# Optimization experiments

Hardware: AMD Instinct MI355X
Metric: run time of the kernel (lower is better)

The kernel has to match this reference:

```python
import jax, jax.numpy as jnp
import numpy as np

W = 128; H = 128; NEAR = 0.1; FAR = 10.0; EPS = 1e-8
B = 1; V = 512; F = 1024


def _perspective(cf, cc):
    # OpenGL-convention projection, returned transposed for row-vector multiply
    f = 0.5 * (cf[0] + cf[1]); pco = 0.5
    right = (W - (cc[0] + pco)) * (NEAR / f)
    left = -(cc[0] + pco) * (NEAR / f)
    top = (cc[1] + pco) * (NEAR / f)
    bottom = -(H - cc[1] + pco) * (NEAR / f)
    z = jnp.zeros(())
    m = jnp.stack([
        jnp.stack([2.0 * NEAR / (right - left), z, (right + left) / (right - left), z]),
        jnp.stack([z, 2.0 * NEAR / (top - bottom), (top + bottom) / (top - bottom), z]),
        jnp.stack([z, z, jnp.full((), -(FAR + NEAR) / (FAR - NEAR)), jnp.full((), -2.0 * FAR * NEAR / (FAR - NEAR))]),
        jnp.stack([z, z, jnp.full((), -1.0), z]),
    ])
    return m.T


def _rodrigues(r):
    theta = jnp.sqrt(jnp.sum(r * r) + 1e-12)
    k = r / theta
    zz = jnp.zeros(())
    K = jnp.stack([
        jnp.stack([zz, -k[2], k[1]]),
        jnp.stack([k[2], zz, -k[0]]),
        jnp.stack([-k[1], k[0], zz]),
    ])
    return jnp.eye(3) + jnp.sin(theta) * K + (1.0 - jnp.cos(theta)) * (K @ K)


def _view_matrix(rt, t):
    # row-vector convention: v' = v @ M, M = rodrigues^T composed with translation-in-last-row
    R = _rodrigues(rt)
    Mr = jnp.eye(4).at[:3, :3].set(R.T)
    Mt = jnp.eye(4).at[3, :3].set(t)
    return Mr @ Mt


def _rasterize_one(vs_xy, z_ndc, inv_w, valid_tri, f, vc, bgcolor, px, py):
    # vs_xy [V,2] screen coords, z_ndc [V], inv_w [V]; f [F,3] int; pixels px,py [P]
    a = vs_xy[f[:, 0]]; b = vs_xy[f[:, 1]]; c = vs_xy[f[:, 2]]  # [F,2]
    x = px[:, None]; y = py[:, None]  # [P,1]
    def E(p, q):  # signed edge function, broadcast to [P,F]
        return (q[:, 0] - p[:, 0]) * (y - p[:, 1]) - (q[:, 1] - p[:, 1]) * (x - p[:, 0])
    w0 = E(b, c); w1 = E(c, a); w2 = E(a, b)  # [P,F]
    area = (b[:, 0] - a[:, 0]) * (c[:, 1] - a[:, 1]) - (b[:, 1] - a[:, 1]) * (c[:, 0] - a[:, 0])  # [F]
    area_safe = jnp.where(jnp.abs(area) > EPS, area, 1.0)
    b0 = w0 / area_safe; b1 = w1 / area_safe; b2 = w2 / area_safe
    za = z_ndc[f[:, 0]]; zb = z_ndc[f[:, 1]]; zc = z_ndc[f[:, 2]]
    z = b0 * za + b1 * zb + b2 * zc  # [P,F] interpolated NDC depth
    inside = ((b0 >= 0) & (b1 >= 0) & (b2 >= 0) & (jnp.abs(area) > EPS)
              & valid_tri[None, :] & (z >= -1.0) & (z <= 1.0))
    depth = jnp.where(inside, z, jnp.inf)
    best = jnp.argmin(depth, axis=1)  # [P] z-buffer winner
    covered = jnp.take_along_axis(depth, best[:, None], 1)[:, 0] <= 1.0
    take = lambda m: jnp.take_along_axis(m, best[:, None], 1)[:, 0]
    bs = jnp.stack([take(b0), take(b1), take(b2)], -1)  # [P,3]
    tri = f[best]          # [P,3]
    iw = inv_w[tri]        # [P,3]
    col = vc[tri]          # [P,3,C]
    den = jnp.sum(bs * iw, -1)
    den = jnp.where(jnp.abs(den) > EPS, den, 1.0)
    color = jnp.einsum('pk,pk,pkc->pc', bs, iw, col) / den[:, None]  # perspective-correct
    return jnp.where(covered[:, None], color, bgcolor[None, :])  # [P,C]


def reference(v, vc, f, bgcolor, camera_f, camera_c, camera_t, camera_rt):
    view = _view_matrix(camera_rt, camera_t)
    proj = _perspective(camera_f, camera_c)
    vh = jnp.concatenate([v, jnp.ones_like(v[..., :1])], -1)  # [B,V,4]
    clip = vh @ (view @ proj)                                 # [B,V,4]
    wc = clip[..., 3]
    valid_v = wc > EPS                                        # in front of camera
    w_safe = jnp.where(valid_v, wc, 1.0)
    ndc = clip[..., :3] / w_safe[..., None]
    xs = (ndc[..., 0] * 0.5 + 0.5) * W
    ys = (0.5 - ndc[..., 1] * 0.5) * H
    vs_xy = jnp.stack([xs, ys], -1)                           # [B,V,2]
    inv_w = 1.0 / w_safe
    valid_tri = valid_v[:, f].all(-1)                         # [B,F]
    gy, gx = jnp.meshgrid(jnp.arange(H, dtype=jnp.float32) + 0.5,
                          jnp.arange(W, dtype=jnp.float32) + 0.5, indexing='ij')
    px = gx.reshape(-1); py = gy.reshape(-1)
    img = jax.vmap(lambda xy, zn, iw, vt: _rasterize_one(xy, zn, iw, vt, f, vc, bgcolor, px, py))(
        vs_xy, ndc[..., 2], inv_w, valid_tri)
    return img.reshape(v.shape[0], H, W, vc.shape[-1])


def setup_inputs() -> dict:
    key = jax.random.key(0)
    k1, k2, k3 = jax.random.split(key, 3)
    u = jax.random.uniform(k1, (B, V, 3), dtype=jnp.float32)
    # x,y in [-0.8,0.8], z in [-3,-1] (camera looks along -z)
    vtx = jnp.stack([u[..., 0] * 1.6 - 0.8, u[..., 1] * 1.6 - 0.8, -(1.0 + 2.0 * u[..., 2])], -1)
    vc = jax.random.uniform(k2, (V, 3), dtype=jnp.float32)
    f = jax.random.randint(k3, (F, 3), 0, V, dtype=jnp.int32)
    return {
        'v': vtx,
        'vc': vc,
        'f': f,
        'bgcolor': jnp.zeros((3,), jnp.float32),
        'camera_f': jnp.array([128.0, 128.0], jnp.float32),
        'camera_c': jnp.array([64.0, 64.0], jnp.float32),
        'camera_t': jnp.zeros((3,), jnp.float32),
        'camera_rt': jnp.zeros((3,), jnp.float32),
    }
```

## Files before the change

kernel.cpp:

```cpp
#include <hip/hip_runtime.h>
#include <math.h>
#include <stdint.h>

#define NV 512
#define NF 1024
#define TRI_STRIDE 16
#define TRI_CHUNK 64
#define NCHUNK (NF / TRI_CHUNK)


__global__ __launch_bounds__(1024) void setup_kernel(
    const float* __restrict__ v, const int* __restrict__ fidx,
    const float* __restrict__ camf, const float* __restrict__ camc,
    const float* __restrict__ camt, const float* __restrict__ camrt,
    double* __restrict__ vdata, double* __restrict__ tridata,
    unsigned long long* __restrict__ keys)
{
#pragma clang fp contract(off)
  __shared__ double sM[16];
  __shared__ double sxs[NV], sys_[NV], szn[NV];
  __shared__ int svld[NV];
  const int tid = threadIdx.x;

  for (int i = tid; i < 16384; i += 1024) keys[i] = ~0ull;

  if (tid == 0) {
    float r0f = camrt[0], r1f = camrt[1], r2f = camrt[2];
    float th = sqrtf(((r0f * r0f + r1f * r1f) + r2f * r2f) + 1e-12f);
    float k0 = r0f / th, k1 = r1f / th, k2 = r2f / th;
    float sthf = sinf(th);
    float cthf = 1.0f - cosf(th);
    double K[3][3] = {{0.0, -(double)k2, (double)k1},
                      {(double)k2, 0.0, -(double)k0},
                      {-(double)k1, (double)k0, 0.0}};
    double KK[3][3];
    for (int i = 0; i < 3; ++i)
      for (int j = 0; j < 3; ++j)
        KK[i][j] = (K[i][0] * K[0][j] + K[i][1] * K[1][j]) + K[i][2] * K[2][j];
    double R[3][3];
    for (int i = 0; i < 3; ++i)
      for (int j = 0; j < 3; ++j) {
        double e = (i == j) ? 1.0 : 0.0;
        R[i][j] = (e + (double)sthf * K[i][j]) + (double)cthf * KK[i][j];
      }
    double Mr[4][4], Mt[4][4];
    for (int i = 0; i < 4; ++i)
      for (int j = 0; j < 4; ++j) {
        Mr[i][j] = (i == j) ? 1.0 : 0.0;
        Mt[i][j] = (i == j) ? 1.0 : 0.0;
      }
    for (int i = 0; i < 3; ++i)
      for (int j = 0; j < 3; ++j) Mr[i][j] = R[j][i];
    Mt[3][0] = (double)camt[0]; Mt[3][1] = (double)camt[1]; Mt[3][2] = (double)camt[2];
    double view[4][4];
    for (int i = 0; i < 4; ++i)
      for (int j = 0; j < 4; ++j)
        view[i][j] = ((Mr[i][0] * Mt[0][j] + Mr[i][1] * Mt[1][j]) +
                      Mr[i][2] * Mt[2][j]) + Mr[i][3] * Mt[3][j];
    float fcam = 0.5f * (camf[0] + camf[1]);
    float nf = 0.1f / fcam;
    float ccx = camc[0], ccy = camc[1];
    float right = (128.0f - (ccx + 0.5f)) * nf;
    float left = -(ccx + 0.5f) * nf;
    float top = (ccy + 0.5f) * nf;
    float bottom = -((128.0f - ccy) + 0.5f) * nf;
    float m00f = 0.2f / (right - left);
    float m02f = (right + left) / (right - left);
    float m11f = 0.2f / (top - bottom);
    float m12f = (top + bottom) / (top - bottom);
    double P[4][4] = {
        {(double)m00f, 0.0, (double)m02f, 0.0},
        {0.0, (double)m11f, (double)m12f, 0.0},
        {0.0, 0.0, -(10.0 + 0.1) / (10.0 - 0.1),
         -2.0 * 10.0 * 0.1 / (10.0 - 0.1)},
        {0.0, 0.0, -1.0, 0.0}};
    for (int i = 0; i < 4; ++i)
      for (int j = 0; j < 4; ++j)
        sM[i * 4 + j] = ((view[i][0] * P[j][0] + view[i][1] * P[j][1]) +
                         view[i][2] * P[j][2]) + view[i][3] * P[j][3];
  }
  __syncthreads();

  if (tid < NV) {
    double x = (double)v[tid * 3 + 0];
    double y = (double)v[tid * 3 + 1];
    double zz = (double)v[tid * 3 + 2];
    double c0 = ((x * sM[0] + y * sM[4]) + zz * sM[8]) + sM[12];
    double c1 = ((x * sM[1] + y * sM[5]) + zz * sM[9]) + sM[13];
    double c2 = ((x * sM[2] + y * sM[6]) + zz * sM[10]) + sM[14];
    double c3 = ((x * sM[3] + y * sM[7]) + zz * sM[11]) + sM[15];
    int valid = c3 > 1e-8;
    double wsafe = valid ? c3 : 1.0;
    double n0 = c0 / wsafe, n1 = c1 / wsafe, n2 = c2 / wsafe;
    double xs = (n0 * 0.5 + 0.5) * 128.0;
    double ys = (0.5 - n1 * 0.5) * 128.0;
    double iw = 1.0 / wsafe;
    sxs[tid] = xs; sys_[tid] = ys; szn[tid] = n2; svld[tid] = valid;
    vdata[0 * NV + tid] = xs;
    vdata[1 * NV + tid] = ys;
    vdata[2 * NV + tid] = n2;
    vdata[3 * NV + tid] = iw;
  }
  __syncthreads();

  {
    int i0 = fidx[tid * 3 + 0], i1 = fidx[tid * 3 + 1], i2 = fidx[tid * 3 + 2];
    double ax = sxs[i0], ay = sys_[i0];
    double bx = sxs[i1], by = sys_[i1];
    double cx = sxs[i2], cy = sys_[i2];
    double p1 = (bx - ax) * (cy - ay);
    double p2 = (by - ay) * (cx - ax);
    double area = p1 - p2;
    bool ok = (fabs(area) > 1e-8) && svld[i0] && svld[i1] && svld[i2];
    double s = (area > 0.0) ? 1.0 : -1.0;
    double inv_abs = ok ? s / area : 1.0;
    double bad = ok ? 0.0 : __builtin_nan("");
    double* td = tridata + tid * TRI_STRIDE;
    td[0] = bx;  td[1] = by;  td[2] = cx;  td[3] = cy;  td[4] = ax;  td[5] = ay;
    td[6] = s * (cx - bx) + bad;  td[7] = s * (cy - by) + bad;
    td[8] = s * (ax - cx) + bad;  td[9] = s * (ay - cy) + bad;
    td[10] = s * (bx - ax) + bad; td[11] = s * (by - ay) + bad;
    td[12] = szn[i0] * inv_abs;
    td[13] = szn[i1] * inv_abs;
    td[14] = szn[i2] * inv_abs;
    td[15] = inv_abs;
  }
}

__global__ __launch_bounds__(256) void raster_kernel(
    const double* __restrict__ tridata, unsigned long long* __restrict__ keys)
{
  __shared__ double st[15][TRI_CHUNK];
  const int tid = threadIdx.x;
  const int chunk = blockIdx.y;
  for (int i = tid; i < 15 * TRI_CHUNK; i += 256) {
    int fld = i >> 6, t = i & 63;
    st[fld][t] = tridata[(chunk * TRI_CHUNK + t) * TRI_STRIDE + fld];
  }
  __syncthreads();

  const int tile = blockIdx.x;
  const int x = ((tile & 7) << 4) + (tid & 15);
  const int y = ((tile >> 3) << 4) + (tid >> 4);
  const double px = (double)x + 0.5, py = (double)y + 0.5;

  double bestz = INFINITY;
  unsigned int bestt = 0;
  for (int t = 0; t < TRI_CHUNK; ++t) {
    double w0 = st[6][t] * (py - st[1][t]) - st[7][t] * (px - st[0][t]);
    double w1 = st[8][t] * (py - st[3][t]) - st[9][t] * (px - st[2][t]);
    double w2 = st[10][t] * (py - st[5][t]) - st[11][t] * (px - st[4][t]);
    double z = (w0 * st[12][t] + w1 * st[13][t]) + w2 * st[14][t];
    bool ins = (w0 >= 0.0) & (w1 >= 0.0) & (w2 >= 0.0) &
               (z >= -1.0) & (z <= 1.0) & (z < bestz);
    if (ins) { bestz = z; bestt = (unsigned int)t; }
  }
  if (bestz < INFINITY) {
    unsigned long long zq = (unsigned long long)((bestz + 1.0) * 4503599627370496.0);
    unsigned long long key = (zq << 10) | (unsigned long long)(chunk * TRI_CHUNK + bestt);
    atomicMin(&keys[y * 128 + x], key);
  }
}

__global__ __launch_bounds__(256) void color_kernel(
    const unsigned long long* __restrict__ keys,
    const double* __restrict__ vdata, const double* __restrict__ tridata,
    const int* __restrict__ fidx, const float* __restrict__ vc,
    const float* __restrict__ bg, float* __restrict__ out)
{
  const int p = blockIdx.x * 256 + threadIdx.x;
  if (p >= 16384) return;
  const int x = p & 127, y = p >> 7;
  unsigned long long key = keys[p];
  float cr, cg, cb;
  if (key == ~0ull) {
    cr = bg[0]; cg = bg[1]; cb = bg[2];
  } else {
    unsigned int t = (unsigned int)(key & 1023ull);
    const double* td = tridata + t * TRI_STRIDE;
    double px = (double)x + 0.5, py = (double)y + 0.5;
    double w0 = td[6] * (py - td[1]) - td[7] * (px - td[0]);
    double w1 = td[8] * (py - td[3]) - td[9] * (px - td[2]);
    double w2 = td[10] * (py - td[5]) - td[11] * (px - td[4]);
    double inv = td[15];
    double b0 = w0 * inv, b1 = w1 * inv, b2 = w2 * inv;
    int i0 = fidx[t * 3 + 0], i1 = fidx[t * 3 + 1], i2 = fidx[t * 3 + 2];
    double t0 = b0 * vdata[3 * NV + i0];
    double t1 = b1 * vdata[3 * NV + i1];
    double t2 = b2 * vdata[3 * NV + i2];
    double den = (t0 + t1) + t2;
    if (!(fabs(den) > 1e-8)) den = 1.0;
    cr = (float)((((t0 * (double)vc[i0 * 3 + 0] + t1 * (double)vc[i1 * 3 + 0]) +
                   t2 * (double)vc[i2 * 3 + 0])) / den);
    cg = (float)((((t0 * (double)vc[i0 * 3 + 1] + t1 * (double)vc[i1 * 3 + 1]) +
                   t2 * (double)vc[i2 * 3 + 1])) / den);
    cb = (float)((((t0 * (double)vc[i0 * 3 + 2] + t1 * (double)vc[i1 * 3 + 2]) +
                   t2 * (double)vc[i2 * 3 + 2])) / den);
  }
  out[p * 3 + 0] = cr;
  out[p * 3 + 1] = cg;
  out[p * 3 + 2] = cb;
}

extern "C" void kernel_launch(void* const* d_in, const int* in_sizes, int n_in,
                              void* d_out, int out_size, void* d_ws, size_t ws_size,
                              hipStream_t stream) {
  const float* v = (const float*)d_in[0];
  const float* vc = (const float*)d_in[1];
  const int* fidx = (const int*)d_in[2];
  const float* bg = (const float*)d_in[3];
  const float* camf = (const float*)d_in[4];
  const float* camc = (const float*)d_in[5];
  const float* camt = (const float*)d_in[6];
  const float* camrt = (const float*)d_in[7];
  float* out = (float*)d_out;

  char* ws = (char*)d_ws;
  unsigned long long* keys = (unsigned long long*)ws;
  double* vdata = (double*)(ws + 131072);
  double* tridata = (double*)(ws + 147456);

  setup_kernel<<<1, 1024, 0, stream>>>(v, fidx, camf, camc, camt, camrt,
                                       vdata, tridata, keys);
  raster_kernel<<<dim3(64, NCHUNK), 256, 0, stream>>>(tridata, keys);
  color_kernel<<<64, 256, 0, stream>>>(keys, vdata, tridata, fidx, vc, bg, out);
}
```

Before: 97.16 us.

## Add float bbox culling and conservative fp32 edge prefilter before fp64 raster test

The setup kernel now also writes a per-triangle float record holding a bounding box, plane-form edge and depth coefficients, and error tolerances. The raster kernel skips triangles whose bbox misses the 16x16 tile and uses cheap fp32 edge and depth tests with conservative margins. It only runs the exact fp64 test when a pixel survives. This removes most fp64 work and the shared-memory staging. It adds scalar loads per triangle and relies on the tolerance bounds being conservative enough to preserve exact results.

Result: slower. 105.2 us (+8.3%).

```diff
diff --git a/kernel.cpp b/kernel.cpp
--- a/kernel.cpp
+++ b/kernel.cpp
@@ -5,6 +5,7 @@
 #define NV 512
 #define NF 1024
 #define TRI_STRIDE 16
+#define TF_STRIDE 20
 #define TRI_CHUNK 64
 #define NCHUNK (NF / TRI_CHUNK)
 
@@ -14,7 +15,7 @@
     const float* __restrict__ camf, const float* __restrict__ camc,
     const float* __restrict__ camt, const float* __restrict__ camrt,
     double* __restrict__ vdata, double* __restrict__ tridata,
-    unsigned long long* __restrict__ keys)
+    float* __restrict__ trifast, unsigned long long* __restrict__ keys)
 {
 #pragma clang fp contract(off)
   __shared__ double sM[16];
@@ -114,50 +115,104 @@
     bool ok = (fabs(area) > 1e-8) && svld[i0] && svld[i1] && svld[i2];
     double s = (area > 0.0) ? 1.0 : -1.0;
     double inv_abs = ok ? s / area : 1.0;
-    double bad = ok ? 0.0 : __builtin_nan("");
+    double kk0 = szn[i0] * inv_abs, kk1 = szn[i1] * inv_abs, kk2 = szn[i2] * inv_abs;
+
     double* td = tridata + tid * TRI_STRIDE;
     td[0] = bx;  td[1] = by;  td[2] = cx;  td[3] = cy;  td[4] = ax;  td[5] = ay;
-    td[6] = s * (cx - bx) + bad;  td[7] = s * (cy - by) + bad;
-    td[8] = s * (ax - cx) + bad;  td[9] = s * (ay - cy) + bad;
-    td[10] = s * (bx - ax) + bad; td[11] = s * (by - ay) + bad;
-    td[12] = szn[i0] * inv_abs;
-    td[13] = szn[i1] * inv_abs;
-    td[14] = szn[i2] * inv_abs;
+    td[6] = s * (cx - bx);  td[7] = s * (cy - by);
+    td[8] = s * (ax - cx);  td[9] = s * (ay - cy);
+    td[10] = s * (bx - ax); td[11] = s * (by - ay);
+    td[12] = kk0; td[13] = kk1; td[14] = kk2;
     td[15] = inv_abs;
+
+    double e0x = cx - bx, e0y = cy - by;
+    double e1x = ax - cx, e1y = ay - cy;
+    double e2x = bx - ax, e2y = by - ay;
+    double A0 = -s * e0y, B0 = s * e0x, C0 = s * (e0y * bx - e0x * by);
+    double A1 = -s * e1y, B1 = s * e1x, C1 = s * (e1y * cx - e1x * cy);
+    double A2 = -s * e2y, B2 = s * e2x, C2 = s * (e2y * ax - e2x * ay);
+    double Az = (A0 * kk0 + A1 * kk1) + A2 * kk2;
+    double Bz = (B0 * kk0 + B1 * kk1) + B2 * kk2;
+    double Cz = (C0 * kk0 + C1 * kk1) + C2 * kk2;
+    double mag0 = (fabs(A0) + fabs(B0)) * 129.0 + fabs(C0);
+    double mag1 = (fabs(A1) + fabs(B1)) * 129.0 + fabs(C1);
+    double mag2 = (fabs(A2) + fabs(B2)) * 129.0 + fabs(C2);
+    double magw = fmax(mag0, fmax(mag1, mag2));
+    double magz = (fabs(Az) + fabs(Bz)) * 129.0 + fabs(Cz);
+    double tw = 9.5367431640625e-07 * magw;
+    double tz = 9.5367431640625e-07 * magz + 1e-6;
+    float bminx, bminy, bmaxx, bmaxy;
+    if (ok) {
+      bminx = (float)(fmin(fmin(ax, bx), cx) - 0.01);
+      bminy = (float)(fmin(fmin(ay, by), cy) - 0.01);
+      bmaxx = (float)(fmax(fmax(ax, bx), cx) + 0.01);
+      bmaxy = (float)(fmax(fmax(ay, by), cy) + 0.01);
+    } else {
+      bminx = 1e30f; bminy = 1e30f; bmaxx = -1e30f; bmaxy = -1e30f;
+    }
+    float* tf = trifast + tid * TF_STRIDE;
+    tf[0] = bminx; tf[1] = bminy; tf[2] = bmaxx; tf[3] = bmaxy;
+    tf[4] = (float)A0; tf[5] = (float)B0; tf[6] = (float)C0;
+    tf[7] = (float)A1; tf[8] = (float)B1; tf[9] = (float)C1;
+    tf[10] = (float)A2; tf[11] = (float)B2; tf[12] = (float)C2;
+    tf[13] = (float)Az; tf[14] = (float)Bz; tf[15] = (float)Cz;
+    tf[16] = (float)tw; tf[17] = (float)tz;
+    tf[18] = 0.0f; tf[19] = 0.0f;
   }
 }
 
 __global__ __launch_bounds__(256) void raster_kernel(
-    const double* __restrict__ tridata, unsigned long long* __restrict__ keys)
+    const float* __restrict__ trifast, const double* __restrict__ tridata,
+    unsigned long long* __restrict__ keys)
 {
-  __shared__ double st[15][TRI_CHUNK];
   const int tid = threadIdx.x;
+  const int tile = blockIdx.x;
   const int chunk = blockIdx.y;
-  for (int i = tid; i < 15 * TRI_CHUNK; i += 256) {
-    int fld = i >> 6, t = i & 63;
-    st[fld][t] = tridata[(chunk * TRI_CHUNK + t) * TRI_STRIDE + fld];
-  }
-  __syncthreads();
-
-  const int tile = blockIdx.x;
-  const int x = ((tile & 7) << 4) + (tid & 15);
-  const int y = ((tile >> 3) << 4) + (tid >> 4);
+  const int x0 = (tile & 7) << 4;
+  const int y0 = (tile >> 3) << 4;
+  const int x = x0 + (tid & 15);
+  const int y = y0 + (tid >> 4);
+  const float pxf = (float)x + 0.5f, pyf = (float)y + 0.5f;
   const double px = (double)x + 0.5, py = (double)y + 0.5;
+  const float txmin = (float)x0 + 0.5f, txmax = (float)x0 + 15.5f;
+  const float tymin = (float)y0 + 0.5f, tymax = (float)y0 + 15.5f;
 
   double bestz = INFINITY;
-  unsigned int bestt = 0;
+  float bestzf = INFINITY;
+  int besti = -1;
+
+  const int tbase = chunk * TRI_CHUNK;
   for (int t = 0; t < TRI_CHUNK; ++t) {
-    double w0 = st[6][t] * (py - st[1][t]) - st[7][t] * (px - st[0][t]);
-    double w1 = st[8][t] * (py - st[3][t]) - st[9][t] * (px - st[2][t]);
-    double w2 = st[10][t] * (py - st[5][t]) - st[11][t] * (px - st[4][t]);
-    double z = (w0 * st[12][t] + w1 * st[13][t]) + w2 * st[14][t];
-    bool ins = (w0 >= 0.0) & (w1 >= 0.0) & (w2 >= 0.0) &
-               (z >= -1.0) & (z <= 1.0) & (z < bestz);
-    if (ins) { bestz = z; bestt = (unsigned int)t; }
-  }
-  if (bestz < INFINITY) {
+    const int tt = __builtin_amdgcn_readfirstlane(tbase + t);
+    const float4* tq = (const float4*)(trifast + tt * TF_STRIDE);
+    float4 q0 = tq[0];
+    if (q0.x > txmax || q0.z < txmin || q0.y > tymax || q0.w < tymin) continue;
+    float4 q1 = tq[1];
+    float4 q2 = tq[2];
+    float4 q3 = tq[3];
+    float4 q4 = tq[4];
+    float w0f = fmaf(q1.x, pxf, fmaf(q1.y, pyf, q1.z));
+    float w1f = fmaf(q1.w, pxf, fmaf(q2.x, pyf, q2.y));
+    float w2f = fmaf(q2.z, pxf, fmaf(q2.w, pyf, q3.x));
+    float zf  = fmaf(q3.y, pxf, fmaf(q3.z, pyf, q3.w));
+    float tw = q4.x, tz = q4.y;
+    float zub = fminf(bestzf, 1.0f) + tz;
+    bool rej = (w0f < -tw) | (w1f < -tw) | (w2f < -tw) |
+               (zf > zub) | (zf < -1.0f - tz);
+    if (!rej) {
+      const double* td = tridata + tt * TRI_STRIDE;
+      double w0 = td[6] * (py - td[1]) - td[7] * (px - td[0]);
+      double w1 = td[8] * (py - td[3]) - td[9] * (px - td[2]);
+      double w2 = td[10] * (py - td[5]) - td[11] * (px - td[4]);
+      double z = (w0 * td[12] + w1 * td[13]) + w2 * td[14];
+      bool ins = (w0 >= 0.0) & (w1 >= 0.0) & (w2 >= 0.0) &
+                 (z >= -1.0) & (z <= 1.0) & (z < bestz);
+      if (ins) { bestz = z; bestzf = (float)z; besti = tt; }
+    }
+  }
+  if (besti >= 0) {
     unsigned long long zq = (unsigned long long)((bestz + 1.0) * 4503599627370496.0);
-    unsigned long long key = (zq << 10) | (unsigned long long)(chunk * TRI_CHUNK + bestt);
+    unsigned long long key = (zq << 10) | (unsigned long long)besti;
     atomicMin(&keys[y * 128 + x], key);
   }
 }
@@ -219,9 +274,10 @@
   unsigned long long* keys = (unsigned long long*)ws;
   double* vdata = (double*)(ws + 131072);
   double* tridata = (double*)(ws + 147456);
+  float* trifast = (float*)(ws + 278528);
 
   setup_kernel<<<1, 1024, 0, stream>>>(v, fidx, camf, camc, camt, camrt,
-                                       vdata, tridata, keys);
-  raster_kernel<<<dim3(64, NCHUNK), 256, 0, stream>>>(tridata, keys);
+                                       vdata, tridata, trifast, keys);
+  raster_kernel<<<dim3(64, NCHUNK), 256, 0, stream>>>(trifast, tridata, keys);
   color_kernel<<<64, 256, 0, stream>>>(keys, vdata, tridata, fidx, vc, bg, out);
 }
```

## Fuse raster and color kernels with bbox culling and affine edge functions

Applied to the files above, without the earlier changes.

The raster and color kernels are merged into one render kernel. The last block to finish for each tile, detected with a per-tile atomic counter, does the shading, which removes one kernel launch. Each block now culls its chunk of triangles against the tile's bounding box using a ballot-compacted list. Edge and depth functions are precomputed as affine coefficients, with w2 derived from the area. This cuts per-triangle work, but adds atomic and fence overhead, and w2 rounding may differ slightly from the direct evaluation.

Result: slower. 113.8 us (+17.1%).

```diff
diff --git a/kernel.cpp b/kernel.cpp
--- a/kernel.cpp
+++ b/kernel.cpp
@@ -5,8 +5,8 @@
 #define NV 512
 #define NF 1024
 #define TRI_STRIDE 16
-#define TRI_CHUNK 64
-#define NCHUNK (NF / TRI_CHUNK)
+#define NGROUP 16
+#define CHUNK 64
 
 
 __global__ __launch_bounds__(1024) void setup_kernel(
@@ -14,7 +14,8 @@
     const float* __restrict__ camf, const float* __restrict__ camc,
     const float* __restrict__ camt, const float* __restrict__ camrt,
     double* __restrict__ vdata, double* __restrict__ tridata,
-    unsigned long long* __restrict__ keys)
+    double* __restrict__ afdata, float4* __restrict__ bbox,
+    unsigned int* __restrict__ done, unsigned long long* __restrict__ keys)
 {
 #pragma clang fp contract(off)
   __shared__ double sM[16];
@@ -23,6 +24,7 @@
   const int tid = threadIdx.x;
 
   for (int i = tid; i < 16384; i += 1024) keys[i] = ~0ull;
+  if (tid < 64) done[tid] = 0u;
 
   if (tid == 0) {
     float r0f = camrt[0], r1f = camrt[1], r2f = camrt[2];
@@ -114,92 +116,143 @@
     bool ok = (fabs(area) > 1e-8) && svld[i0] && svld[i1] && svld[i2];
     double s = (area > 0.0) ? 1.0 : -1.0;
     double inv_abs = ok ? s / area : 1.0;
-    double bad = ok ? 0.0 : __builtin_nan("");
+    double kk0 = szn[i0] * inv_abs, kk1 = szn[i1] * inv_abs, kk2 = szn[i2] * inv_abs;
+
     double* td = tridata + tid * TRI_STRIDE;
     td[0] = bx;  td[1] = by;  td[2] = cx;  td[3] = cy;  td[4] = ax;  td[5] = ay;
-    td[6] = s * (cx - bx) + bad;  td[7] = s * (cy - by) + bad;
-    td[8] = s * (ax - cx) + bad;  td[9] = s * (ay - cy) + bad;
-    td[10] = s * (bx - ax) + bad; td[11] = s * (by - ay) + bad;
-    td[12] = szn[i0] * inv_abs;
-    td[13] = szn[i1] * inv_abs;
-    td[14] = szn[i2] * inv_abs;
+    td[6] = s * (cx - bx);  td[7] = s * (cy - by);
+    td[8] = s * (ax - cx);  td[9] = s * (ay - cy);
+    td[10] = s * (bx - ax); td[11] = s * (by - ay);
+    td[12] = kk0; td[13] = kk1; td[14] = kk2;
     td[15] = inv_abs;
+
+    double e0x = cx - bx, e0y = cy - by;
+    double e1x = ax - cx, e1y = ay - cy;
+    double e2x = bx - ax, e2y = by - ay;
+    double A0 = -s * e0y, B0 = s * e0x, C0 = s * (e0y * bx - e0x * by);
+    double A1 = -s * e1y, B1 = s * e1x, C1 = s * (e1y * cx - e1x * cy);
+    double A2 = -s * e2y, B2 = s * e2x, C2 = s * (e2y * ax - e2x * ay);
+    double Az = (A0 * kk0 + A1 * kk1) + A2 * kk2;
+    double Bz = (B0 * kk0 + B1 * kk1) + B2 * kk2;
+    double Cz = (C0 * kk0 + C1 * kk1) + C2 * kk2;
+    double* af = afdata + tid * 10;
+    af[0] = A0; af[1] = B0; af[2] = C0;
+    af[3] = A1; af[4] = B1; af[5] = C1;
+    af[6] = Az; af[7] = Bz; af[8] = Cz;
+    af[9] = ok ? (s * area) : __builtin_nan("");
+
+    float4 bb;
+    if (ok) {
+      bb.x = (float)(fmin(fmin(ax, bx), cx) - 0.01);
+      bb.y = (float)(fmin(fmin(ay, by), cy) - 0.01);
+      bb.z = (float)(fmax(fmax(ax, bx), cx) + 0.01);
+      bb.w = (float)(fmax(fmax(ay, by), cy) + 0.01);
+    } else {
+      bb.x = 1e30f; bb.y = 1e30f; bb.z = -1e30f; bb.w = -1e30f;
+    }
+    bbox[tid] = bb;
   }
 }
 
-__global__ __launch_bounds__(256) void raster_kernel(
-    const double* __restrict__ tridata, unsigned long long* __restrict__ keys)
+__global__ __launch_bounds__(256) void render_kernel(
+    const double* __restrict__ afdata, const float4* __restrict__ bbox,
+    const double* __restrict__ tridata, const double* __restrict__ vdata,
+    const int* __restrict__ fidx, const float* __restrict__ vc,
+    const float* __restrict__ bg, unsigned long long* __restrict__ keys,
+    unsigned int* __restrict__ done, float* __restrict__ out)
 {
-  __shared__ double st[15][TRI_CHUNK];
+  __shared__ double sc[CHUNK][10];
+  __shared__ int slist[CHUNK];
+  __shared__ int scnt;
+  __shared__ int s_last;
   const int tid = threadIdx.x;
-  const int chunk = blockIdx.y;
-  for (int i = tid; i < 15 * TRI_CHUNK; i += 256) {
-    int fld = i >> 6, t = i & 63;
-    st[fld][t] = tridata[(chunk * TRI_CHUNK + t) * TRI_STRIDE + fld];
-  }
-  __syncthreads();
-
   const int tile = blockIdx.x;
-  const int x = ((tile & 7) << 4) + (tid & 15);
-  const int y = ((tile >> 3) << 4) + (tid >> 4);
+  const int group = blockIdx.y;
+  const int x0 = (tile & 7) << 4;
+  const int y0 = (tile >> 3) << 4;
+  const int x = x0 + (tid & 15);
+  const int y = y0 + (tid >> 4);
+  const int tbase = group * CHUNK;
+
+  {
+    const float* src = (const float*)(afdata + (size_t)tbase * 10);
+    float* dst = (float*)sc;
+    for (int i = tid; i < CHUNK * 10 * 2; i += 256) dst[i] = src[i];
+  }
+  if (tid < 64) {
+    float4 bb = bbox[tbase + tid];
+    const float txmin = (float)x0 + 0.5f, txmax = (float)x0 + 15.5f;
+    const float tymin = (float)y0 + 0.5f, tymax = (float)y0 + 15.5f;
+    bool hit = !(bb.x > txmax || bb.z < txmin || bb.y > tymax || bb.w < tymin);
+    unsigned long long m = __ballot(hit);
+    int pos = __popcll(m & ((1ull << tid) - 1ull));
+    if (hit) slist[pos] = tid;
+    if (tid == 0) scnt = (int)__popcll(m);
+  }
+  __syncthreads();
+
+  const int cnt = scnt;
   const double px = (double)x + 0.5, py = (double)y + 0.5;
-
   double bestz = INFINITY;
-  unsigned int bestt = 0;
-  for (int t = 0; t < TRI_CHUNK; ++t) {
-    double w0 = st[6][t] * (py - st[1][t]) - st[7][t] * (px - st[0][t]);
-    double w1 = st[8][t] * (py - st[3][t]) - st[9][t] * (px - st[2][t]);
-    double w2 = st[10][t] * (py - st[5][t]) - st[11][t] * (px - st[4][t]);
-    double z = (w0 * st[12][t] + w1 * st[13][t]) + w2 * st[14][t];
+  int besti = -1;
+  for (int j = 0; j < cnt; ++j) {
+    int t = slist[j];
+    const double* c = sc[t];
+    double w0 = (c[0] * px + c[1] * py) + c[2];
+    double w1 = (c[3] * px + c[4] * py) + c[5];
+    double z  = (c[6] * px + c[7] * py) + c[8];
+    double w2 = (c[9] - w0) - w1;
     bool ins = (w0 >= 0.0) & (w1 >= 0.0) & (w2 >= 0.0) &
                (z >= -1.0) & (z <= 1.0) & (z < bestz);
-    if (ins) { bestz = z; bestt = (unsigned int)t; }
-  }
-  if (bestz < INFINITY) {
+    bestz = ins ? z : bestz;
+    besti = ins ? (tbase + t) : besti;
+  }
+  if (besti >= 0) {
     unsigned long long zq = (unsigned long long)((bestz + 1.0) * 4503599627370496.0);
-    unsigned long long key = (zq << 10) | (unsigned long long)(chunk * TRI_CHUNK + bestt);
-    atomicMin(&keys[y * 128 + x], key);
-  }
-}
-
-__global__ __launch_bounds__(256) void color_kernel(
-    const unsigned long long* __restrict__ keys,
-    const double* __restrict__ vdata, const double* __restrict__ tridata,
-    const int* __restrict__ fidx, const float* __restrict__ vc,
-    const float* __restrict__ bg, float* __restrict__ out)
-{
-  const int p = blockIdx.x * 256 + threadIdx.x;
-  if (p >= 16384) return;
-  const int x = p & 127, y = p >> 7;
-  unsigned long long key = keys[p];
-  float cr, cg, cb;
-  if (key == ~0ull) {
-    cr = bg[0]; cg = bg[1]; cb = bg[2];
-  } else {
-    unsigned int t = (unsigned int)(key & 1023ull);
-    const double* td = tridata + t * TRI_STRIDE;
-    double px = (double)x + 0.5, py = (double)y + 0.5;
-    double w0 = td[6] * (py - td[1]) - td[7] * (px - td[0]);
-    double w1 = td[8] * (py - td[3]) - td[9] * (px - td[2]);
-    double w2 = td[10] * (py - td[5]) - td[11] * (px - td[4]);
-    double inv = td[15];
-    double b0 = w0 * inv, b1 = w1 * inv, b2 = w2 * inv;
-    int i0 = fidx[t * 3 + 0], i1 = fidx[t * 3 + 1], i2 = fidx[t * 3 + 2];
-    double t0 = b0 * vdata[3 * NV + i0];
-    double t1 = b1 * vdata[3 * NV + i1];
-    double t2 = b2 * vdata[3 * NV + i2];
-    double den = (t0 + t1) + t2;
-    if (!(fabs(den) > 1e-8)) den = 1.0;
-    cr = (float)((((t0 * (double)vc[i0 * 3 + 0] + t1 * (double)vc[i1 * 3 + 0]) +
-                   t2 * (double)vc[i2 * 3 + 0])) / den);
-    cg = (float)((((t0 * (double)vc[i0 * 3 + 1] + t1 * (double)vc[i1 * 3 + 1]) +
-                   t2 * (double)vc[i2 * 3 + 1])) / den);
-    cb = (float)((((t0 * (double)vc[i0 * 3 + 2] + t1 * (double)vc[i1 * 3 + 2]) +
-                   t2 * (double)vc[i2 * 3 + 2])) / den);
-  }
-  out[p * 3 + 0] = cr;
-  out[p * 3 + 1] = cg;
-  out[p * 3 + 2] = cb;
+    atomicMin(&keys[y * 128 + x], (zq << 10) | (unsigned long long)besti);
+  }
+
+  __syncthreads();
+  if (tid == 0) {
+    __threadfence();
+    unsigned int old = __hip_atomic_fetch_add(&done[tile], 1u, __ATOMIC_ACQ_REL,
+                                              __HIP_MEMORY_SCOPE_AGENT);
+    s_last = (old == NGROUP - 1) ? 1 : 0;
+  }
+  __syncthreads();
+
+  if (s_last) {
+    const int p = y * 128 + x;
+    unsigned long long key = __hip_atomic_load(&keys[p], __ATOMIC_RELAXED,
+                                               __HIP_MEMORY_SCOPE_AGENT);
+    float cr, cg, cb;
+    if (key == ~0ull) {
+      cr = bg[0]; cg = bg[1]; cb = bg[2];
+    } else {
+      unsigned int t = (unsigned int)(key & 1023ull);
+      const double* td = tridata + t * TRI_STRIDE;
+      double w0 = td[6] * (py - td[1]) - td[7] * (px - td[0]);
+      double w1 = td[8] * (py - td[3]) - td[9] * (px - td[2]);
+      double w2 = td[10] * (py - td[5]) - td[11] * (px - td[4]);
+      double inv = td[15];
+      double b0 = w0 * inv, b1 = w1 * inv, b2 = w2 * inv;
+      int i0 = fidx[t * 3 + 0], i1 = fidx[t * 3 + 1], i2 = fidx[t * 3 + 2];
+      double t0 = b0 * vdata[3 * NV + i0];
+      double t1 = b1 * vdata[3 * NV + i1];
+      double t2 = b2 * vdata[3 * NV + i2];
+      double den = (t0 + t1) + t2;
+      if (!(fabs(den) > 1e-8)) den = 1.0;
+      cr = (float)((((t0 * (double)vc[i0 * 3 + 0] + t1 * (double)vc[i1 * 3 + 0]) +
+                     t2 * (double)vc[i2 * 3 + 0])) / den);
+      cg = (float)((((t0 * (double)vc[i0 * 3 + 1] + t1 * (double)vc[i1 * 3 + 1]) +
+                     t2 * (double)vc[i2 * 3 + 1])) / den);
+      cb = (float)((((t0 * (double)vc[i0 * 3 + 2] + t1 * (double)vc[i1 * 3 + 2]) +
+                     t2 * (double)vc[i2 * 3 + 2])) / den);
+    }
+    out[p * 3 + 0] = cr;
+    out[p * 3 + 1] = cg;
+    out[p * 3 + 2] = cb;
+  }
 }
 
 extern "C" void kernel_launch(void* const* d_in, const int* in_sizes, int n_in,
@@ -219,9 +272,12 @@
   unsigned long long* keys = (unsigned long long*)ws;
   double* vdata = (double*)(ws + 131072);
   double* tridata = (double*)(ws + 147456);
+  double* afdata = (double*)(ws + 278528);
+  float4* bbox = (float4*)(ws + 360448);
+  unsigned int* done = (unsigned int*)(ws + 376832);
 
   setup_kernel<<<1, 1024, 0, stream>>>(v, fidx, camf, camc, camt, camrt,
-                                       vdata, tridata, keys);
-  raster_kernel<<<dim3(64, NCHUNK), 256, 0, stream>>>(tridata, keys);
-  color_kernel<<<64, 256, 0, stream>>>(keys, vdata, tridata, fidx, vc, bg, out);
+                                       vdata, tridata, afdata, bbox, done, keys);
+  render_kernel<<<dim3(64, NGROUP), 256, 0, stream>>>(
+      afdata, bbox, tridata, vdata, fidx, vc, bg, keys, done, out);
 }
```

## Precompute affine edge and depth coefficients per triangle for rasterization

Applied to the files above, without the earlier changes.

Setup now turns each triangle's edge functions and interpolated depth into affine plane equations (A*px + B*py + C) and packs them into double2 arrays. The raster loop then costs three affine evaluations and a subtraction, with w2 taken from the total area, instead of three edge products plus a depth dot product. The loop is unrolled by four and uses select-based updates. Reformulating the arithmetic may change rounding at edges and depth ties compared with the original edge-function form, and invalid triangles are now rejected through a NaN area term.

New measurement: 93.05 us. 4.2% less time.

```diff
diff --git a/kernel.cpp b/kernel.cpp
--- a/kernel.cpp
+++ b/kernel.cpp
@@ -5,8 +5,8 @@
 #define NV 512
 #define NF 1024
 #define TRI_STRIDE 16
-#define TRI_CHUNK 64
-#define NCHUNK (NF / TRI_CHUNK)
+#define NGROUP 16
+#define CHUNK 64
 
 
 __global__ __launch_bounds__(1024) void setup_kernel(
@@ -14,7 +14,7 @@
     const float* __restrict__ camf, const float* __restrict__ camc,
     const float* __restrict__ camt, const float* __restrict__ camrt,
     double* __restrict__ vdata, double* __restrict__ tridata,
-    unsigned long long* __restrict__ keys)
+    double2* __restrict__ afT, unsigned long long* __restrict__ keys)
 {
 #pragma clang fp contract(off)
   __shared__ double sM[16];
@@ -114,51 +114,74 @@
     bool ok = (fabs(area) > 1e-8) && svld[i0] && svld[i1] && svld[i2];
     double s = (area > 0.0) ? 1.0 : -1.0;
     double inv_abs = ok ? s / area : 1.0;
-    double bad = ok ? 0.0 : __builtin_nan("");
+    double kk0 = szn[i0] * inv_abs, kk1 = szn[i1] * inv_abs, kk2 = szn[i2] * inv_abs;
+
     double* td = tridata + tid * TRI_STRIDE;
     td[0] = bx;  td[1] = by;  td[2] = cx;  td[3] = cy;  td[4] = ax;  td[5] = ay;
-    td[6] = s * (cx - bx) + bad;  td[7] = s * (cy - by) + bad;
-    td[8] = s * (ax - cx) + bad;  td[9] = s * (ay - cy) + bad;
-    td[10] = s * (bx - ax) + bad; td[11] = s * (by - ay) + bad;
-    td[12] = szn[i0] * inv_abs;
-    td[13] = szn[i1] * inv_abs;
-    td[14] = szn[i2] * inv_abs;
+    td[6] = s * (cx - bx);  td[7] = s * (cy - by);
+    td[8] = s * (ax - cx);  td[9] = s * (ay - cy);
+    td[10] = s * (bx - ax); td[11] = s * (by - ay);
+    td[12] = kk0; td[13] = kk1; td[14] = kk2;
     td[15] = inv_abs;
+
+    double e0x = cx - bx, e0y = cy - by;
+    double e1x = ax - cx, e1y = ay - cy;
+    double e2x = bx - ax, e2y = by - ay;
+    double A0 = -s * e0y, B0 = s * e0x, C0 = s * (e0y * bx - e0x * by);
+    double A1 = -s * e1y, B1 = s * e1x, C1 = s * (e1y * cx - e1x * cy);
+    double A2 = -s * e2y, B2 = s * e2x, C2 = s * (e2y * ax - e2x * ay);
+    double Az = (A0 * kk0 + A1 * kk1) + A2 * kk2;
+    double Bz = (B0 * kk0 + B1 * kk1) + B2 * kk2;
+    double Cz = (C0 * kk0 + C1 * kk1) + C2 * kk2;
+    double absarea = ok ? (s * area) : __builtin_nan("");
+    afT[0 * NF + tid] = make_double2(A0, B0);
+    afT[1 * NF + tid] = make_double2(C0, A1);
+    afT[2 * NF + tid] = make_double2(B1, C1);
+    afT[3 * NF + tid] = make_double2(Az, Bz);
+    afT[4 * NF + tid] = make_double2(Cz, absarea);
   }
 }
 
 __global__ __launch_bounds__(256) void raster_kernel(
-    const double* __restrict__ tridata, unsigned long long* __restrict__ keys)
+    const double2* __restrict__ afT, unsigned long long* __restrict__ keys)
 {
-  __shared__ double st[15][TRI_CHUNK];
+  __shared__ double2 sc[5][CHUNK];
   const int tid = threadIdx.x;
-  const int chunk = blockIdx.y;
-  for (int i = tid; i < 15 * TRI_CHUNK; i += 256) {
-    int fld = i >> 6, t = i & 63;
-    st[fld][t] = tridata[(chunk * TRI_CHUNK + t) * TRI_STRIDE + fld];
+  const int tile = blockIdx.x;
+  const int group = blockIdx.y;
+  const int tbase = group * CHUNK;
+
+  for (int i = tid; i < 5 * CHUNK; i += 256) {
+    int f = i >> 6, t = i & 63;
+    sc[f][t] = afT[f * NF + tbase + t];
   }
   __syncthreads();
 
-  const int tile = blockIdx.x;
   const int x = ((tile & 7) << 4) + (tid & 15);
   const int y = ((tile >> 3) << 4) + (tid >> 4);
   const double px = (double)x + 0.5, py = (double)y + 0.5;
 
   double bestz = INFINITY;
-  unsigned int bestt = 0;
-  for (int t = 0; t < TRI_CHUNK; ++t) {
-    double w0 = st[6][t] * (py - st[1][t]) - st[7][t] * (px - st[0][t]);
-    double w1 = st[8][t] * (py - st[3][t]) - st[9][t] * (px - st[2][t]);
-    double w2 = st[10][t] * (py - st[5][t]) - st[11][t] * (px - st[4][t]);
-    double z = (w0 * st[12][t] + w1 * st[13][t]) + w2 * st[14][t];
+  int besti = -1;
+#pragma unroll 4
+  for (int t = 0; t < CHUNK; ++t) {
+    double2 c0 = sc[0][t];
+    double2 c1 = sc[1][t];
+    double2 c2 = sc[2][t];
+    double2 c3 = sc[3][t];
+    double2 c4 = sc[4][t];
+    double w0 = (c0.x * px + c0.y * py) + c1.x;
+    double w1 = (c1.y * px + c2.x * py) + c2.y;
+    double z  = (c3.x * px + c3.y * py) + c4.x;
+    double w2 = (c4.y - w0) - w1;
     bool ins = (w0 >= 0.0) & (w1 >= 0.0) & (w2 >= 0.0) &
                (z >= -1.0) & (z <= 1.0) & (z < bestz);
-    if (ins) { bestz = z; bestt = (unsigned int)t; }
-  }
-  if (bestz < INFINITY) {
+    bestz = ins ? z : bestz;
+    besti = ins ? (tbase + t) : besti;
+  }
+  if (besti >= 0) {
     unsigned long long zq = (unsigned long long)((bestz + 1.0) * 4503599627370496.0);
-    unsigned long long key = (zq << 10) | (unsigned long long)(chunk * TRI_CHUNK + bestt);
-    atomicMin(&keys[y * 128 + x], key);
+    atomicMin(&keys[y * 128 + x], (zq << 10) | (unsigned long long)besti);
   }
 }
 
@@ -219,9 +242,10 @@
   unsigned long long* keys = (unsigned long long*)ws;
   double* vdata = (double*)(ws + 131072);
   double* tridata = (double*)(ws + 147456);
+  double2* afT = (double2*)(ws + 278528);
 
   setup_kernel<<<1, 1024, 0, stream>>>(v, fidx, camf, camc, camt, camrt,
-                                       vdata, tridata, keys);
-  raster_kernel<<<dim3(64, NCHUNK), 256, 0, stream>>>(tridata, keys);
+                                       vdata, tridata, afT, keys);
+  raster_kernel<<<dim3(64, NGROUP), 256, 0, stream>>>(afT, keys);
   color_kernel<<<64, 256, 0, stream>>>(keys, vdata, tridata, fidx, vc, bg, out);
 }
```
